# Kernel tuning notes

Hardware: AMD Instinct MI355X
Metric: run time of the kernel (lower is better)

Reference implementation:

```python
import jax, jax.numpy as jnp
import numpy as np

N_NODES = 100000


def gcn_layer(x, src, dst, W, b, num_nodes):
    """PyG GCNConv: out = D^-1/2 (A + I) D^-1/2 (x W) + b, with self-loops."""
    h = x @ W  # [N, out_dim]
    # add self-loops
    loop = jnp.arange(num_nodes, dtype=src.dtype)
    s = jnp.concatenate([src, loop])
    d = jnp.concatenate([dst, loop])
    # symmetric normalization (degree counted on destination, incl. self-loops)
    deg = jax.ops.segment_sum(jnp.ones_like(d, dtype=h.dtype), d, num_segments=num_nodes)
    dinv = jnp.where(deg > 0, jax.lax.rsqrt(deg), 0.0)
    norm = dinv[s] * dinv[d]  # [E+N]
    # gather -> weight -> scatter-add
    msg = h[s] * norm[:, None]  # [E+N, out_dim]
    out = jax.ops.segment_sum(msg, d, num_segments=num_nodes)
    return out + b


def setup_inputs() -> dict:
    key = jax.random.key(0)
    k1, k2, k3, k4 = jax.random.split(key, 4)
    in_chan, h1, h2 = 256, 128, 64
    n_edges = 1600000
    x = jax.random.normal(k1, (N_NODES, in_chan), dtype=jnp.float32)
    edge_index = jax.random.randint(k2, (2, n_edges), 0, N_NODES, dtype=jnp.int64)
    W1 = jax.random.normal(k3, (in_chan, h1), dtype=jnp.float32) * (1.0 / np.sqrt(in_chan))
    b1 = jnp.zeros((h1,), dtype=jnp.float32)
    W2 = jax.random.normal(k4, (h1, h2), dtype=jnp.float32) * (1.0 / np.sqrt(h1))
    b2 = jnp.zeros((h2,), dtype=jnp.float32)
    return {"x": x, "edge_index": edge_index, "W1": W1, "b1": b1, "W2": W2, "b2": b2}


def reference(x, edge_index, W1, b1, W2, b2):
    src, dst = edge_index[0], edge_index[1]
    h = jax.nn.relu(gcn_layer(x, src, dst, W1, b1, N_NODES))
    return jax.nn.relu(gcn_layer(h, src, dst, W2, b2, N_NODES))
```

## Files before the change

kernel.cpp:

```cpp
#include <hip/hip_runtime.h>
#include <hip/hip_fp16.h>

#define NNODES 100000

#define OFF_W1TH     0UL
#define OFF_W1TL     65536UL
#define OFF_W2TH     131072UL
#define OFF_W2TL     147456UL
#define OFF_BCNT     163840UL
#define OFF_BBASE    165888UL
#define OFF_BCUR     167936UL
#define OFF_ROWPTR   400128UL
#define OFF_DINV     1200640UL
#define OFF_COL      1605632UL
#define OFF_EBUF     8005632UL
#define OFF_H1G      8005632UL
#define OFF_H1OUT    59205632UL

typedef __attribute__((ext_vector_type(8))) _Float16 f16x8;
typedef __attribute__((ext_vector_type(4))) float f32x4;

__device__ __forceinline__ void async_copy16(void* lds, const void* g) {
    __builtin_amdgcn_global_load_lds(
        (const __attribute__((address_space(1))) unsigned*)g,
        (__attribute__((address_space(3))) unsigned*)lds, 16, 0, 0);
}

__global__ __launch_bounds__(256) void bincount(const int* __restrict__ dst,
                                                int* __restrict__ bcnt, int E) {
    __shared__ int lc[512];
    int t = threadIdx.x;
    lc[t] = 0; lc[t + 256] = 0;
    __syncthreads();
    for (int e = blockIdx.x * 256 + t; e < E; e += gridDim.x * 256)
        atomicAdd(&lc[dst[e] >> 8], 1);
    __syncthreads();
    if (lc[t]) atomicAdd(&bcnt[t], lc[t]);
    if (lc[t + 256]) atomicAdd(&bcnt[t + 256], lc[t + 256]);
}

__global__ __launch_bounds__(512) void bscan(const int* __restrict__ bcnt,
                                             int* __restrict__ bbase,
                                             int* __restrict__ bcur,
                                             int* __restrict__ rowptr,
                                             int NB, int N, int E) {
    __shared__ int s[512];
    int t = threadIdx.x;
    int v = (t < NB) ? bcnt[t] : 0;
    s[t] = v;
    __syncthreads();
    for (int off = 1; off < 512; off <<= 1) {
        int add = (t >= off) ? s[t - off] : 0;
        __syncthreads();
        s[t] += add;
        __syncthreads();
    }
    if (t < NB) {
        int ex = s[t] - v;
        bbase[t] = ex;
        bcur[t] = ex;
    }
    if (t == 0) rowptr[N] = E;
}

#define CHUNK 8192
__global__ __launch_bounds__(256) void binscatter(const int* __restrict__ src,
                                                  const int* __restrict__ dst,
                                                  int* __restrict__ bcur,
                                                  int* __restrict__ ebuf, int E) {
    __shared__ int lc[512];
    __shared__ int gb[512];
    int t = threadIdx.x;
    lc[t] = 0; lc[t + 256] = 0;
    __syncthreads();
    int base = blockIdx.x * CHUNK;
    int rb[32];
#pragma unroll
    for (int i = 0; i < 32; ++i) {
        int e = base + i * 256 + t;
        if (e < E) {
            int b = dst[e] >> 8;
            rb[i] = (b << 13) | atomicAdd(&lc[b], 1);
        } else rb[i] = -1;
    }
    __syncthreads();
    if (lc[t]) gb[t] = atomicAdd(&bcur[t], lc[t]);
    if (lc[t + 256]) gb[t + 256] = atomicAdd(&bcur[t + 256], lc[t + 256]);
    __syncthreads();
#pragma unroll
    for (int i = 0; i < 32; ++i) {
        if (rb[i] >= 0) {
            int e = base + i * 256 + t;
            int b = rb[i] >> 13, r = rb[i] & 8191;
            ebuf[gb[b] + r] = src[e] | ((dst[e] & 255) << 20);
        }
    }
}

__global__ __launch_bounds__(256) void buildcsr(const int* __restrict__ ebuf,
                                                const int* __restrict__ bbase,
                                                const int* __restrict__ bcnt,
                                                int* __restrict__ rowptr,
                                                int* __restrict__ colarr,
                                                float* __restrict__ dinv, int N) {
    int b = blockIdx.x;
    int t = threadIdx.x;
    int start = bbase[b];
    int cnt = bcnt[b];
    __shared__ int nc[256];
    __shared__ int s[256];
    __shared__ int ncur[256];
    nc[t] = 0;
    __syncthreads();
    for (int e = t; e < cnt; e += 256) atomicAdd(&nc[ebuf[start + e] >> 20], 1);
    __syncthreads();
    int own = nc[t];
    s[t] = own;
    __syncthreads();
    for (int off = 1; off < 256; off <<= 1) {
        int add = (t >= off) ? s[t - off] : 0;
        __syncthreads();
        s[t] += add;
        __syncthreads();
    }
    int rowbase = start + s[t] - own;
    int n0 = b << 8;
    if (n0 + t < N) {
        rowptr[n0 + t] = rowbase;
        dinv[n0 + t] = rsqrtf((float)(own + 1));
    }
    ncur[t] = rowbase;
    __syncthreads();
    for (int e = t; e < cnt; e += 256) {
        int pe = ebuf[start + e];
        int slot = atomicAdd(&ncur[pe >> 20], 1);
        colarr[slot] = pe & 0xFFFFF;
    }
}

__global__ __launch_bounds__(256) void split_wt_frag(const float* __restrict__ W,
                                                     _Float16* __restrict__ hi,
                                                     _Float16* __restrict__ lo,
                                                     int K, int N) {
    int idx = blockIdx.x * 256 + threadIdx.x;
    if (idx >= K * N) return;
    int NT = N >> 4;
    int j = idx & 7;
    int l = (idx >> 3) & 63;
    int f = idx >> 9;
    int nt = f % NT;
    int kc = f / NT;
    int k = kc * 32 + (l >> 4) * 8 + j;
    int n = nt * 16 + (l & 15);
    float v = W[k * N + n];
    _Float16 h = (_Float16)v;
    hi[idx] = h;
    lo[idx] = (_Float16)(v - (float)h);
}

template <int BN, int KTOT, bool AFP16>
__global__ __launch_bounds__(256, 3) void gemm_f16(const void* __restrict__ Araw,
                                                   const _Float16* __restrict__ Bh_g,
                                                   const _Float16* __restrict__ Bl_g,
                                                   const float* __restrict__ dinv,
                                                   _Float16* __restrict__ C, int M) {
    constexpr int NT = BN / 16;
    constexpr int NK = KTOT / 32;
    constexpr int TILE = NT * 512;
    constexpr int FPW = NT / 4;
    __shared__ _Float16 Bsh[2][TILE];
    __shared__ _Float16 Bsl[2][TILE];

    const int tid = threadIdx.x;
    const int wave = tid >> 6;
    const int lane = tid & 63;
    const int lm = lane & 15;
    const int q = lane >> 4;
    const int m0 = blockIdx.x * 128;

    const int r0 = m0 + wave * 32 + lm;
    const int r1 = r0 + 16;
    const bool vr0 = r0 < M;
    const bool vr1 = r1 < M;

    const float* Af = (const float*)Araw;
    const _Float16* Ah16 = (const _Float16*)Araw;

    f32x4 acc[2][NT];
#pragma unroll
    for (int a = 0; a < 2; ++a)
#pragma unroll
        for (int b = 0; b < NT; ++b) acc[a][b] = (f32x4){0.f, 0.f, 0.f, 0.f};

    float4 pa0, pa1, pa2, pa3;
    uint4 ph0, ph1;

#define STAGE_B(kc_, b_)                                                          \
    do {                                                                          \
        _Pragma("unroll")                                                         \
        for (int i_ = 0; i_ < FPW; ++i_) {                                        \
            int f_ = wave * FPW + i_;                                             \
            async_copy16(&Bsh[b_][f_ * 512 + lane * 8],                           \
                         Bh_g + (size_t)(kc_) * TILE + f_ * 512 + lane * 8);      \
            async_copy16(&Bsl[b_][f_ * 512 + lane * 8],                           \
                         Bl_g + (size_t)(kc_) * TILE + f_ * 512 + lane * 8);      \
        }                                                                         \
    } while (0)

#define LOAD_A(t_)                                                                \
    do {                                                                          \
        const int k_ = (t_) * 32 + q * 8;                                         \
        if (AFP16) {                                                              \
            ph0 = vr0 ? *(const uint4*)&Ah16[(size_t)r0 * KTOT + k_]              \
                      : make_uint4(0u, 0u, 0u, 0u);                               \
            ph1 = vr1 ? *(const uint4*)&Ah16[(size_t)r1 * KTOT + k_]              \
                      : make_uint4(0u, 0u, 0u, 0u);                               \
        } else {                                                                  \
            float4 z_ = make_float4(0.f, 0.f, 0.f, 0.f);                          \
            pa0 = vr0 ? *(const float4*)&Af[(size_t)r0 * KTOT + k_] : z_;         \
            pa1 = vr0 ? *(const float4*)&Af[(size_t)r0 * KTOT + k_ + 4] : z_;     \
            pa2 = vr1 ? *(const float4*)&Af[(size_t)r1 * KTOT + k_] : z_;         \
            pa3 = vr1 ? *(const float4*)&Af[(size_t)r1 * KTOT + k_ + 4] : z_;     \
        }                                                                         \
    } while (0)

    STAGE_B(0, 0);
    LOAD_A(0);
    __syncthreads();

#pragma unroll
    for (int t = 0; t < NK; ++t) {
        const int b = t & 1;
        if (t + 1 < NK) STAGE_B(t + 1, b ^ 1);

        f16x8 a0, a1;
        if (AFP16) {
            a0 = *(f16x8*)&ph0;
            a1 = *(f16x8*)&ph1;
        } else {
            a0[0] = (_Float16)pa0.x; a0[1] = (_Float16)pa0.y;
            a0[2] = (_Float16)pa0.z; a0[3] = (_Float16)pa0.w;
            a0[4] = (_Float16)pa1.x; a0[5] = (_Float16)pa1.y;
            a0[6] = (_Float16)pa1.z; a0[7] = (_Float16)pa1.w;
            a1[0] = (_Float16)pa2.x; a1[1] = (_Float16)pa2.y;
            a1[2] = (_Float16)pa2.z; a1[3] = (_Float16)pa2.w;
            a1[4] = (_Float16)pa3.x; a1[5] = (_Float16)pa3.y;
            a1[6] = (_Float16)pa3.z; a1[7] = (_Float16)pa3.w;
        }
        if (t + 1 < NK) LOAD_A(t + 1);

#pragma unroll
        for (int nt = 0; nt < NT; ++nt) {
            f16x8 bh = *(const f16x8*)&Bsh[b][nt * 512 + lane * 8];
            f16x8 bl = *(const f16x8*)&Bsl[b][nt * 512 + lane * 8];
            acc[0][nt] = __builtin_amdgcn_mfma_f32_16x16x32_f16(a0, bh, acc[0][nt], 0, 0, 0);
            acc[0][nt] = __builtin_amdgcn_mfma_f32_16x16x32_f16(a0, bl, acc[0][nt], 0, 0, 0);
            acc[1][nt] = __builtin_amdgcn_mfma_f32_16x16x32_f16(a1, bh, acc[1][nt], 0, 0, 0);
            acc[1][nt] = __builtin_amdgcn_mfma_f32_16x16x32_f16(a1, bl, acc[1][nt], 0, 0, 0);
        }
        if (t + 1 < NK) __syncthreads();
    }
#undef STAGE_B
#undef LOAD_A

#pragma unroll
    for (int mt = 0; mt < 2; ++mt) {
#pragma unroll
        for (int i = 0; i < 4; ++i) {
            int r = m0 + wave * 32 + mt * 16 + q * 4 + i;
            if (r < M) {
                float dv = dinv[r];
#pragma unroll
                for (int nt = 0; nt < NT; ++nt) {
                    C[(size_t)r * BN + nt * 16 + lm] = (_Float16)(acc[mt][nt][i] * dv);
                }
            }
        }
    }
}

__device__ __forceinline__ void acc8(float* a, uint4 v) {
    float2 f0 = __half22float2(*(const __half2*)&v.x);
    float2 f1 = __half22float2(*(const __half2*)&v.y);
    float2 f2 = __half22float2(*(const __half2*)&v.z);
    float2 f3 = __half22float2(*(const __half2*)&v.w);
    a[0] += f0.x; a[1] += f0.y; a[2] += f1.x; a[3] += f1.y;
    a[4] += f2.x; a[5] += f2.y; a[6] += f3.x; a[7] += f3.y;
}

__global__ __launch_bounds__(256) void agg128(const _Float16* __restrict__ g,
                                              const int* __restrict__ rowptr,
                                              const int* __restrict__ colarr,
                                              const float* __restrict__ dinv,
                                              const float* __restrict__ bias,
                                              _Float16* __restrict__ out, int n) {
    int node = blockIdx.x * 4 + (threadIdx.x >> 6);
    int lane = threadIdx.x & 63;
    if (node >= n) return;
    int sel = lane >> 4;
    int co = (lane & 15) << 3;

    int beg = rowptr[node];
    int end = rowptr[node + 1];

    float a[8] = {0.f, 0.f, 0.f, 0.f, 0.f, 0.f, 0.f, 0.f};
    if (sel == 0) acc8(a, *(const uint4*)&g[(node << 7) + co]);

    int p = beg;
    for (; p + 16 <= end; p += 16) {
        int r0 = colarr[p + sel];
        int r1 = colarr[p + 4 + sel];
        int r2 = colarr[p + 8 + sel];
        int r3 = colarr[p + 12 + sel];
        uint4 v0 = *(const uint4*)&g[(r0 << 7) + co];
        uint4 v1 = *(const uint4*)&g[(r1 << 7) + co];
        uint4 v2 = *(const uint4*)&g[(r2 << 7) + co];
        uint4 v3 = *(const uint4*)&g[(r3 << 7) + co];
        acc8(a, v0); acc8(a, v1); acc8(a, v2); acc8(a, v3);
    }
    for (; p + 4 <= end; p += 4) {
        int r = colarr[p + sel];
        acc8(a, *(const uint4*)&g[(r << 7) + co]);
    }
    int rem = end - p;
    if (sel < rem) {
        int r = colarr[p + sel];
        acc8(a, *(const uint4*)&g[(r << 7) + co]);
    }

#pragma unroll
    for (int i = 0; i < 8; ++i) {
        a[i] += __shfl(a[i], lane ^ 16);
        a[i] += __shfl(a[i], lane ^ 32);
    }

    if (sel == 0) {
        float dv = dinv[node];
        float4 b0 = *(const float4*)&bias[co];
        float4 b1 = *(const float4*)&bias[co + 4];
        float o0 = fmaxf(fmaf(a[0], dv, b0.x), 0.f);
        float o1 = fmaxf(fmaf(a[1], dv, b0.y), 0.f);
        float o2 = fmaxf(fmaf(a[2], dv, b0.z), 0.f);
        float o3 = fmaxf(fmaf(a[3], dv, b0.w), 0.f);
        float o4 = fmaxf(fmaf(a[4], dv, b1.x), 0.f);
        float o5 = fmaxf(fmaf(a[5], dv, b1.y), 0.f);
        float o6 = fmaxf(fmaf(a[6], dv, b1.z), 0.f);
        float o7 = fmaxf(fmaf(a[7], dv, b1.w), 0.f);
        __half2 h0 = __floats2half2_rn(o0, o1);
        __half2 h1 = __floats2half2_rn(o2, o3);
        __half2 h2 = __floats2half2_rn(o4, o5);
        __half2 h3 = __floats2half2_rn(o6, o7);
        uint4 pk = make_uint4(*(unsigned*)&h0, *(unsigned*)&h1,
                              *(unsigned*)&h2, *(unsigned*)&h3);
        *(uint4*)&out[(node << 7) + co] = pk;
    }
}

__global__ __launch_bounds__(256) void agg64(const _Float16* __restrict__ g,
                                             const int* __restrict__ rowptr,
                                             const int* __restrict__ colarr,
                                             const float* __restrict__ dinv,
                                             const float* __restrict__ bias,
                                             float* __restrict__ out, int n) {
    int node = blockIdx.x * 4 + (threadIdx.x >> 6);
    int lane = threadIdx.x & 63;
    if (node >= n) return;
    int sel = lane >> 3;
    int co = (lane & 7) << 3;

    int beg = rowptr[node];
    int end = rowptr[node + 1];

    float a[8] = {0.f, 0.f, 0.f, 0.f, 0.f, 0.f, 0.f, 0.f};
    if (sel == 0) acc8(a, *(const uint4*)&g[(node << 6) + co]);

    int p = beg;
    for (; p + 16 <= end; p += 16) {
        int r0 = colarr[p + sel];
        int r1 = colarr[p + 8 + sel];
        uint4 v0 = *(const uint4*)&g[(r0 << 6) + co];
        uint4 v1 = *(const uint4*)&g[(r1 << 6) + co];
        acc8(a, v0); acc8(a, v1);
    }
    for (; p + 8 <= end; p += 8) {
        int r = colarr[p + sel];
        acc8(a, *(const uint4*)&g[(r << 6) + co]);
    }
    int rem = end - p;
    if (sel < rem) {
        int r = colarr[p + sel];
        acc8(a, *(const uint4*)&g[(r << 6) + co]);
    }

#pragma unroll
    for (int i = 0; i < 8; ++i) {
        a[i] += __shfl(a[i], lane ^ 8);
        a[i] += __shfl(a[i], lane ^ 16);
        a[i] += __shfl(a[i], lane ^ 32);
    }

    if (sel == 0) {
        float dv = dinv[node];
        float4 b0 = *(const float4*)&bias[co];
        float4 b1 = *(const float4*)&bias[co + 4];
        float4 oA, oB;
        oA.x = fmaxf(fmaf(a[0], dv, b0.x), 0.f);
        oA.y = fmaxf(fmaf(a[1], dv, b0.y), 0.f);
        oA.z = fmaxf(fmaf(a[2], dv, b0.z), 0.f);
        oA.w = fmaxf(fmaf(a[3], dv, b0.w), 0.f);
        oB.x = fmaxf(fmaf(a[4], dv, b1.x), 0.f);
        oB.y = fmaxf(fmaf(a[5], dv, b1.y), 0.f);
        oB.z = fmaxf(fmaf(a[6], dv, b1.z), 0.f);
        oB.w = fmaxf(fmaf(a[7], dv, b1.w), 0.f);
        *(float4*)&out[(node << 6) + co] = oA;
        *(float4*)&out[(node << 6) + co + 4] = oB;
    }
}

extern "C" void kernel_launch(void* const* d_in, const int* in_sizes, int n_in,
                              void* d_out, int out_size, void* d_ws, size_t ws_size,
                              hipStream_t stream) {
    const float* x  = (const float*)d_in[0];
    const int*   ei = (const int*)d_in[1];
    const float* W1 = (const float*)d_in[2];
    const float* b1 = (const float*)d_in[3];
    const float* W2 = (const float*)d_in[4];
    const float* b2 = (const float*)d_in[5];
    float* out = (float*)d_out;

    const int E = in_sizes[1] / 2;
    const int H1 = in_sizes[3];
    const int K1 = in_sizes[2] / H1;
    const int N = in_sizes[0] / K1;
    const int H2 = in_sizes[4] / H1;
    const int* src = ei;
    const int* dst = ei + E;
    const int NB = (N + 255) >> 8;

    char* ws = (char*)d_ws;
    _Float16* w1th   = (_Float16*)(ws + OFF_W1TH);
    _Float16* w1tl   = (_Float16*)(ws + OFF_W1TL);
    _Float16* w2th   = (_Float16*)(ws + OFF_W2TH);
    _Float16* w2tl   = (_Float16*)(ws + OFF_W2TL);
    int*      bcnt   = (int*)(ws + OFF_BCNT);
    int*      bbase  = (int*)(ws + OFF_BBASE);
    int*      bcur   = (int*)(ws + OFF_BCUR);
    int*      rowptr = (int*)(ws + OFF_ROWPTR);
    float*    dinv   = (float*)(ws + OFF_DINV);
    int*      colarr = (int*)(ws + OFF_COL);
    int*      ebuf   = (int*)(ws + OFF_EBUF);
    _Float16* h1g    = (_Float16*)(ws + OFF_H1G);
    _Float16* h1out  = (_Float16*)(ws + OFF_H1OUT);
    _Float16* h2g    = (_Float16*)(ws + OFF_H1G);

    hipMemsetAsync(bcnt, 0, 512 * sizeof(int), stream);
    bincount<<<256, 256, 0, stream>>>(dst, bcnt, E);
    bscan<<<1, 512, 0, stream>>>(bcnt, bbase, bcur, rowptr, NB, N, E);
    binscatter<<<(E + CHUNK - 1) / CHUNK, 256, 0, stream>>>(src, dst, bcur, ebuf, E);
    buildcsr<<<NB, 256, 0, stream>>>(ebuf, bbase, bcnt, rowptr, colarr, dinv, N);

    split_wt_frag<<<(K1 * H1 + 255) / 256, 256, 0, stream>>>(W1, w1th, w1tl, K1, H1);
    split_wt_frag<<<(H1 * H2 + 255) / 256, 256, 0, stream>>>(W2, w2th, w2tl, H1, H2);

    gemm_f16<128, 256, false><<<(N + 127) / 128, 256, 0, stream>>>(x, w1th, w1tl, dinv, h1g, N);
    agg128<<<(N + 3) / 4, 256, 0, stream>>>(h1g, rowptr, colarr, dinv, b1, h1out, N);

    gemm_f16<64, 128, true><<<(N + 127) / 128, 256, 0, stream>>>(h1out, w2th, w2tl, dinv, h2g, N);
    agg64<<<(N + 3) / 4, 256, 0, stream>>>(h2g, rowptr, colarr, dinv, b2, out, N);
}
```

Before: 417.1 us.

## Stage multi-k-chunk B phases in LDS and double-buffer A register prefetch

The GEMM no longer double-buffers one 32-wide k-chunk of B per iteration with a barrier each step. It now loads several k-chunks (up to 32/NT) of the hi/lo B fragments into LDS at once and needs only one barrier per phase. A-operand loads are prefetched two chunks ahead through alternating register sets, to hide global latency better. The cost is larger LDS use and more registers, and launch_bounds drops the min-blocks hint, which may lower occupancy.

```diff
diff --git a/kernel.cpp b/kernel.cpp
--- a/kernel.cpp
+++ b/kernel.cpp
@@ -159,17 +159,19 @@
 }
 
 template <int BN, int KTOT, bool AFP16>
-__global__ __launch_bounds__(256, 3) void gemm_f16(const void* __restrict__ Araw,
-                                                   const _Float16* __restrict__ Bh_g,
-                                                   const _Float16* __restrict__ Bl_g,
-                                                   const float* __restrict__ dinv,
-                                                   _Float16* __restrict__ C, int M) {
+__global__ __launch_bounds__(256) void gemm_f16(const void* __restrict__ Araw,
+                                                const _Float16* __restrict__ Bh_g,
+                                                const _Float16* __restrict__ Bl_g,
+                                                const float* __restrict__ dinv,
+                                                _Float16* __restrict__ C, int M) {
     constexpr int NT = BN / 16;
     constexpr int NK = KTOT / 32;
+    constexpr int KPP = (NK < (32 / NT)) ? NK : (32 / NT);
+    constexpr int NPH = NK / KPP;
     constexpr int TILE = NT * 512;
-    constexpr int FPW = NT / 4;
-    __shared__ _Float16 Bsh[2][TILE];
-    __shared__ _Float16 Bsl[2][TILE];
+    constexpr int CH = (KPP * TILE) / (256 * 8);
+    __shared__ _Float16 Bsh[KPP * TILE];
+    __shared__ _Float16 Bsl[KPP * TILE];
 
     const int tid = threadIdx.x;
     const int wave = tid >> 6;
@@ -192,76 +194,83 @@
 #pragma unroll
         for (int b = 0; b < NT; ++b) acc[a][b] = (f32x4){0.f, 0.f, 0.f, 0.f};
 
-    float4 pa0, pa1, pa2, pa3;
-    uint4 ph0, ph1;
-
-#define STAGE_B(kc_, b_)                                                          \
-    do {                                                                          \
-        _Pragma("unroll")                                                         \
-        for (int i_ = 0; i_ < FPW; ++i_) {                                        \
-            int f_ = wave * FPW + i_;                                             \
-            async_copy16(&Bsh[b_][f_ * 512 + lane * 8],                           \
-                         Bh_g + (size_t)(kc_) * TILE + f_ * 512 + lane * 8);      \
-            async_copy16(&Bsl[b_][f_ * 512 + lane * 8],                           \
-                         Bl_g + (size_t)(kc_) * TILE + f_ * 512 + lane * 8);      \
-        }                                                                         \
+    const float4 fz_ = make_float4(0.f, 0.f, 0.f, 0.f);
+    const uint4 uz_ = make_uint4(0u, 0u, 0u, 0u);
+
+    float4 pA0, pA1, pA2, pA3, pB0, pB1, pB2, pB3;
+    uint4 hA0, hA1, hB0, hB1;
+
+#define LOAD_SET(p0_, p1_, p2_, p3_, h0_, h1_, t_)                                 \
+    do {                                                                           \
+        const int k_ = (t_) * 32 + q * 8;                                          \
+        if (AFP16) {                                                               \
+            h0_ = vr0 ? *(const uint4*)&Ah16[(size_t)r0 * KTOT + k_] : uz_;        \
+            h1_ = vr1 ? *(const uint4*)&Ah16[(size_t)r1 * KTOT + k_] : uz_;        \
+        } else {                                                                   \
+            p0_ = vr0 ? *(const float4*)&Af[(size_t)r0 * KTOT + k_] : fz_;         \
+            p1_ = vr0 ? *(const float4*)&Af[(size_t)r0 * KTOT + k_ + 4] : fz_;     \
+            p2_ = vr1 ? *(const float4*)&Af[(size_t)r1 * KTOT + k_] : fz_;         \
+            p3_ = vr1 ? *(const float4*)&Af[(size_t)r1 * KTOT + k_ + 4] : fz_;     \
+        }                                                                          \
     } while (0)
 
-#define LOAD_A(t_)                                                                \
-    do {                                                                          \
-        const int k_ = (t_) * 32 + q * 8;                                         \
-        if (AFP16) {                                                              \
-            ph0 = vr0 ? *(const uint4*)&Ah16[(size_t)r0 * KTOT + k_]              \
-                      : make_uint4(0u, 0u, 0u, 0u);                               \
-            ph1 = vr1 ? *(const uint4*)&Ah16[(size_t)r1 * KTOT + k_]              \
-                      : make_uint4(0u, 0u, 0u, 0u);                               \
-        } else {                                                                  \
-            float4 z_ = make_float4(0.f, 0.f, 0.f, 0.f);                          \
-            pa0 = vr0 ? *(const float4*)&Af[(size_t)r0 * KTOT + k_] : z_;         \
-            pa1 = vr0 ? *(const float4*)&Af[(size_t)r0 * KTOT + k_ + 4] : z_;     \
-            pa2 = vr1 ? *(const float4*)&Af[(size_t)r1 * KTOT + k_] : z_;         \
-            pa3 = vr1 ? *(const float4*)&Af[(size_t)r1 * KTOT + k_ + 4] : z_;     \
-        }                                                                         \
+#define CONV_SET(a0_, a1_, p0_, p1_, p2_, p3_, h0_, h1_)                           \
+    do {                                                                           \
+        if (AFP16) {                                                               \
+            a0_ = *(f16x8*)&h0_;                                                   \
+            a1_ = *(f16x8*)&h1_;                                                   \
+        } else {                                                                   \
+            a0_[0] = (_Float16)p0_.x; a0_[1] = (_Float16)p0_.y;                    \
+            a0_[2] = (_Float16)p0_.z; a0_[3] = (_Float16)p0_.w;                    \
+            a0_[4] = (_Float16)p1_.x; a0_[5] = (_Float16)p1_.y;                    \
+            a0_[6] = (_Float16)p1_.z; a0_[7] = (_Float16)p1_.w;                    \
+            a1_[0] = (_Float16)p2_.x; a1_[1] = (_Float16)p2_.y;                    \
+            a1_[2] = (_Float16)p2_.z; a1_[3] = (_Float16)p2_.w;                    \
+            a1_[4] = (_Float16)p3_.x; a1_[5] = (_Float16)p3_.y;                    \
+            a1_[6] = (_Float16)p3_.z; a1_[7] = (_Float16)p3_.w;                    \
+        }                                                                          \
     } while (0)
 
-    STAGE_B(0, 0);
-    LOAD_A(0);
-    __syncthreads();
-
-#pragma unroll
-    for (int t = 0; t < NK; ++t) {
-        const int b = t & 1;
-        if (t + 1 < NK) STAGE_B(t + 1, b ^ 1);
-
-        f16x8 a0, a1;
-        if (AFP16) {
-            a0 = *(f16x8*)&ph0;
-            a1 = *(f16x8*)&ph1;
-        } else {
-            a0[0] = (_Float16)pa0.x; a0[1] = (_Float16)pa0.y;
-            a0[2] = (_Float16)pa0.z; a0[3] = (_Float16)pa0.w;
-            a0[4] = (_Float16)pa1.x; a0[5] = (_Float16)pa1.y;
-            a0[6] = (_Float16)pa1.z; a0[7] = (_Float16)pa1.w;
-            a1[0] = (_Float16)pa2.x; a1[1] = (_Float16)pa2.y;
-            a1[2] = (_Float16)pa2.z; a1[3] = (_Float16)pa2.w;
-            a1[4] = (_Float16)pa3.x; a1[5] = (_Float16)pa3.y;
-            a1[6] = (_Float16)pa3.z; a1[7] = (_Float16)pa3.w;
+    LOAD_SET(pA0, pA1, pA2, pA3, hA0, hA1, 0);
+    if (NK > 1) LOAD_SET(pB0, pB1, pB2, pB3, hB0, hB1, 1);
+
+#pragma unroll
+    for (int ph = 0; ph < NPH; ++ph) {
+        const _Float16* bh_g = Bh_g + (size_t)ph * KPP * TILE;
+        const _Float16* bl_g = Bl_g + (size_t)ph * KPP * TILE;
+#pragma unroll
+        for (int i = 0; i < CH; ++i) {
+            int c = (i * 256 + tid) * 8;
+            async_copy16(&Bsh[c], bh_g + c);
+            async_copy16(&Bsl[c], bl_g + c);
         }
-        if (t + 1 < NK) LOAD_A(t + 1);
-
-#pragma unroll
-        for (int nt = 0; nt < NT; ++nt) {
-            f16x8 bh = *(const f16x8*)&Bsh[b][nt * 512 + lane * 8];
-            f16x8 bl = *(const f16x8*)&Bsl[b][nt * 512 + lane * 8];
-            acc[0][nt] = __builtin_amdgcn_mfma_f32_16x16x32_f16(a0, bh, acc[0][nt], 0, 0, 0);
-            acc[0][nt] = __builtin_amdgcn_mfma_f32_16x16x32_f16(a0, bl, acc[0][nt], 0, 0, 0);
-            acc[1][nt] = __builtin_amdgcn_mfma_f32_16x16x32_f16(a1, bh, acc[1][nt], 0, 0, 0);
-            acc[1][nt] = __builtin_amdgcn_mfma_f32_16x16x32_f16(a1, bl, acc[1][nt], 0, 0, 0);
+        __syncthreads();
+
+#pragma unroll
+        for (int t = 0; t < KPP; ++t) {
+            const int g = ph * KPP + t;
+            f16x8 a0, a1;
+            if ((g & 1) == 0) {
+                CONV_SET(a0, a1, pA0, pA1, pA2, pA3, hA0, hA1);
+                if (g + 2 < NK) LOAD_SET(pA0, pA1, pA2, pA3, hA0, hA1, g + 2);
+            } else {
+                CONV_SET(a0, a1, pB0, pB1, pB2, pB3, hB0, hB1);
+                if (g + 2 < NK) LOAD_SET(pB0, pB1, pB2, pB3, hB0, hB1, g + 2);
+            }
+#pragma unroll
+            for (int nt = 0; nt < NT; ++nt) {
+                f16x8 bh = *(const f16x8*)&Bsh[(t * NT + nt) * 512 + lane * 8];
+                f16x8 bl = *(const f16x8*)&Bsl[(t * NT + nt) * 512 + lane * 8];
+                acc[0][nt] = __builtin_amdgcn_mfma_f32_16x16x32_f16(a0, bh, acc[0][nt], 0, 0, 0);
+                acc[0][nt] = __builtin_amdgcn_mfma_f32_16x16x32_f16(a0, bl, acc[0][nt], 0, 0, 0);
+                acc[1][nt] = __builtin_amdgcn_mfma_f32_16x16x32_f16(a1, bh, acc[1][nt], 0, 0, 0);
+                acc[1][nt] = __builtin_amdgcn_mfma_f32_16x16x32_f16(a1, bl, acc[1][nt], 0, 0, 0);
+            }
         }
-        if (t + 1 < NK) __syncthreads();
-    }
-#undef STAGE_B
-#undef LOAD_A
+        if (ph + 1 < NPH) __syncthreads();
+    }
+#undef LOAD_SET
+#undef CONV_SET
 
 #pragma unroll
     for (int mt = 0; mt < 2; ++mt) {
```

Result: no change. 417.5 us (+0.1%).
